# Performance work log

Hardware: AMD Instinct MI355X
Metric: run time of the kernel (lower is better)

## Reference

```python
import jax, jax.numpy as jnp
import numpy as np

B, N, L, ND = 512, 4096, 128, 1


def setup_inputs() -> dict:
    key = jax.random.key(0)
    ks = jax.random.split(key, 20)
    g = lambda k, shape, s=0.05: jax.random.normal(k, shape, dtype=jnp.float32) * s
    IN = 3 * L + ND  # MLP input: [mem, mem, delta_t, x]
    inp = {
        "x": jax.random.normal(ks[0], (B, N, ND), jnp.float32),
        "memory": jax.random.normal(ks[1], (N, L), jnp.float32),
        "delta_t": jax.random.normal(ks[2], (B, N, L), jnp.float32),
        "src_w1": g(ks[3], (L, IN)), "src_b1": g(ks[4], (L,)),
        "src_w2": g(ks[5], (L, L)), "src_b2": g(ks[6], (L,)),
        "tar_w1": g(ks[7], (L, IN)), "tar_b1": g(ks[8], (L,)),
        "tar_w2": g(ks[9], (L, L)), "tar_b2": g(ks[10], (L,)),
        "gru_wih": g(ks[11], (3 * L, L)), "gru_whh": g(ks[12], (3 * L, L)),
        "gru_bih": g(ks[13], (3 * L,)), "gru_bhh": g(ks[14], (3 * L,)),
        "source": jax.random.randint(ks[15], (B, 1), 0, N, dtype=jnp.int64),
        "target": jax.random.randint(ks[16], (B, 1), 0, N, dtype=jnp.int64),
    }
    return inp


def _mlp(h, w1, b1, w2, b2):
    return jax.nn.relu(h @ w1.T + b1) @ w2.T + b2


def _gru_cell(inp, h, wih, whh, bih, bhh):
    gi = inp @ wih.T + bih          # [n, 3L]
    gh = h @ whh.T + bhh            # [n, 3L]
    i_r, i_z, i_n = jnp.split(gi, 3, axis=-1)
    h_r, h_z, h_n = jnp.split(gh, 3, axis=-1)
    r = jax.nn.sigmoid(i_r + h_r)
    z = jax.nn.sigmoid(i_z + h_z)
    n = jnp.tanh(i_n + r * h_n)
    return (1.0 - z) * n + z * h


def reference(x, memory, delta_t, src_w1, src_b1, src_w2, src_b2,
              tar_w1, tar_b1, tar_w2, tar_b2,
              gru_wih, gru_whh, gru_bih, gru_bhh, source, target):
    b = x.shape[0]
    bi = jnp.arange(b)
    s = source[:, 0]
    t = target[:, 0]
    src_mem = memory[s]                 # [B, L]
    tar_mem = memory[t]                 # [B, L]
    src_x = x[bi, s, :]                 # [B, ND]
    tar_x = x[bi, t, :]
    src_dt = delta_t[bi, s, :]          # [B, L]
    tar_dt = delta_t[bi, t, :]
    src_in = jnp.concatenate([src_mem, tar_mem, src_dt, src_x], axis=-1)
    tar_in = jnp.concatenate([tar_mem, src_mem, tar_dt, tar_x], axis=-1)
    src_msg = _mlp(src_in, src_w1, src_b1, src_w2, src_b2)
    tar_msg = _mlp(tar_in, tar_w1, tar_b1, tar_w2, tar_b2)

    # unique + scatter_mean == segment-mean over node ids, touching only seen nodes
    ids = jnp.concatenate([s, t], axis=0)                       # [2B]
    msgs = jnp.concatenate([src_msg, tar_msg], axis=0)          # [2B, L]
    n_nodes = memory.shape[0]
    msg_sum = jax.ops.segment_sum(msgs, ids, num_segments=n_nodes)
    cnt = jax.ops.segment_sum(jnp.ones((ids.shape[0],), msgs.dtype), ids,
                              num_segments=n_nodes)
    agg = msg_sum / jnp.maximum(cnt, 1.0)[:, None]              # [N, L]
    new_mem = _gru_cell(agg, memory, gru_wih, gru_whh, gru_bih, gru_bhh)
    seen = (cnt > 0)[:, None]
    return jnp.where(seen, new_mem, memory)
```

## Files before the change

### kernel.cpp

```cpp
#include <hip/hip_runtime.h>
#include <math.h>

#define BB 512
#define NN 4096
#define LL 128
#define IN_DIM 385
#define IN_PAD 388
#define NK4_1 97
#define NK4_2 32
#define EPB 2
#define GPB 4

#define OFF_MSG   0
#define OFF_CNT   (OFF_MSG + NN * LL)
#define OFF_COUNT (OFF_CNT + NN)
#define OFF_LIST  (OFF_COUNT + 4)
#define OFF_W1PS  529416
#define OFF_W1PT  (OFF_W1PS + NK4_1 * LL * 4)
#define OFF_W2PS  (OFF_W1PT + NK4_1 * LL * 4)
#define OFF_W2PT  (OFF_W2PS + NK4_2 * LL * 4)
#define OFF_WIHP  (OFF_W2PT + NK4_2 * LL * 4)
#define OFF_WHHP  (OFF_WIHP + 3 * NK4_2 * LL * 4)

__global__ __launch_bounds__(256) void prep_kernel(
    const float* __restrict__ memory,
    const float* __restrict__ sw1, const float* __restrict__ tw1,
    const float* __restrict__ sw2, const float* __restrict__ tw2,
    const float* __restrict__ wih, const float* __restrict__ whh,
    float* __restrict__ ws, float* __restrict__ out)
{
    const int i = blockIdx.x * 256 + threadIdx.x;
    const int stride = gridDim.x * 256;

    float4* out4 = (float4*)out;
    const float4* mem4 = (const float4*)memory;
    float4* msg4 = (float4*)(ws + OFF_MSG);
    const float4 z4 = make_float4(0.f, 0.f, 0.f, 0.f);
    for (int idx = i; idx < NN * LL / 4; idx += stride) {
        out4[idx] = mem4[idx];
        msg4[idx] = z4;
    }
    for (int idx = i; idx < NN; idx += stride)
        ws[OFF_CNT + idx] = 0.0f;
    if (i == 0)
        ((int*)ws)[OFF_COUNT] = 0;

    float4* w1ps = (float4*)(ws + OFF_W1PS);
    float4* w1pt = (float4*)(ws + OFF_W1PT);
    for (int idx = i; idx < NK4_1 * LL; idx += stride) {
        const int k4 = idx >> 7, j = idx & 127;
        const int k = k4 * 4;
        float4 a, b;
        a.x = sw1[j * IN_DIM + k];     b.x = tw1[j * IN_DIM + k];
        a.y = sw1[j * IN_DIM + k + 1]; b.y = tw1[j * IN_DIM + k + 1];
        a.z = sw1[j * IN_DIM + k + 2]; b.z = tw1[j * IN_DIM + k + 2];
        if (k + 3 < IN_DIM) { a.w = sw1[j * IN_DIM + k + 3]; b.w = tw1[j * IN_DIM + k + 3]; }
        else                { a.w = 0.f; b.w = 0.f; }
        if (k + 2 >= IN_DIM) { a.z = 0.f; b.z = 0.f; }
        if (k + 1 >= IN_DIM) { a.y = 0.f; b.y = 0.f; }
        w1ps[idx] = a; w1pt[idx] = b;
    }
    float4* w2ps = (float4*)(ws + OFF_W2PS);
    float4* w2pt = (float4*)(ws + OFF_W2PT);
    for (int idx = i; idx < NK4_2 * LL; idx += stride) {
        const int k4 = idx >> 7, j = idx & 127;
        const int k = k4 * 4;
        w2ps[idx] = make_float4(sw2[j * LL + k], sw2[j * LL + k + 1],
                                sw2[j * LL + k + 2], sw2[j * LL + k + 3]);
        w2pt[idx] = make_float4(tw2[j * LL + k], tw2[j * LL + k + 1],
                                tw2[j * LL + k + 2], tw2[j * LL + k + 3]);
    }
    float4* wihp = (float4*)(ws + OFF_WIHP);
    float4* whhp = (float4*)(ws + OFF_WHHP);
    for (int idx = i; idx < 3 * NK4_2 * LL; idx += stride) {
        const int j = idx & 127;
        const int gk = idx >> 7;
        const int gate = gk >> 5, k4 = gk & 31;
        const int row = gate * LL + j, k = k4 * 4;
        wihp[idx] = make_float4(wih[row * LL + k], wih[row * LL + k + 1],
                                wih[row * LL + k + 2], wih[row * LL + k + 3]);
        whhp[idx] = make_float4(whh[row * LL + k], whh[row * LL + k + 1],
                                whh[row * LL + k + 2], whh[row * LL + k + 3]);
    }
}

__global__ __launch_bounds__(256) void edge_msg_kernel(
    const float* __restrict__ x,
    const float* __restrict__ memory,
    const float* __restrict__ delta_t,
    const float* __restrict__ sb1, const float* __restrict__ sb2,
    const float* __restrict__ tb1, const float* __restrict__ tb2,
    const int* __restrict__ source, const int* __restrict__ target,
    float* __restrict__ ws)
{
    const int side  = blockIdx.x & 1;
    const int chunk = blockIdx.x >> 1;
    const int tid   = threadIdx.x;
    const int g     = tid >> 7;
    const int j     = tid & 127;

    __shared__ float in2[IN_PAD][EPB];
    __shared__ float h1[LL][EPB];
    __shared__ float part1[2][EPB][LL];
    __shared__ float part2[2][EPB][LL];
    __shared__ int   node_sh[EPB];

    const float4* w1p = (const float4*)(ws + (side ? OFF_W1PT : OFF_W1PS));
    const float4* w2p = (const float4*)(ws + (side ? OFF_W2PT : OFF_W2PS));
    const float* b1  = side ? tb1 : sb1;
    const float* b2  = side ? tb2 : sb2;

    #pragma unroll
    for (int e = 0; e < EPB; ++e) {
        const int eg = chunk * EPB + e;
        const int s = source[eg], t = target[eg];
        const int node  = side ? t : s;
        const int other = side ? s : t;
        if (tid == 0) node_sh[e] = node;
        for (int idx = tid; idx < IN_PAD; idx += 256) {
            float v = 0.0f;
            if (idx < LL)           v = memory[node * LL + idx];
            else if (idx < 2 * LL)  v = memory[other * LL + (idx - LL)];
            else if (idx < 3 * LL)  v = delta_t[((size_t)eg * NN + node) * LL + (idx - 2 * LL)];
            else if (idx == 3 * LL) v = x[(size_t)eg * NN + node];
            in2[idx][e] = v;
        }
    }
    __syncthreads();

    {
        const int k40 = g ? 49 : 0;
        const int k41 = g ? NK4_1 : 49;
        float a0 = 0.f, a1 = 0.f;
        #pragma unroll 4
        for (int k4 = k40; k4 < k41; ++k4) {
            const float4 w  = w1p[k4 * LL + j];
            const float4 i0 = *(const float4*)&in2[k4 * 4][0];
            const float4 i1 = *(const float4*)&in2[k4 * 4 + 2][0];
            a0 = fmaf(w.x, i0.x, a0); a1 = fmaf(w.x, i0.y, a1);
            a0 = fmaf(w.y, i0.z, a0); a1 = fmaf(w.y, i0.w, a1);
            a0 = fmaf(w.z, i1.x, a0); a1 = fmaf(w.z, i1.y, a1);
            a0 = fmaf(w.w, i1.z, a0); a1 = fmaf(w.w, i1.w, a1);
        }
        part1[g][0][j] = a0;
        part1[g][1][j] = a1;
    }
    __syncthreads();

    h1[j][g] = fmaxf(part1[0][g][j] + part1[1][g][j] + b1[j], 0.0f);
    __syncthreads();

    {
        const int k40 = g * 16, k41 = k40 + 16;
        float a0 = 0.f, a1 = 0.f;
        #pragma unroll 4
        for (int k4 = k40; k4 < k41; ++k4) {
            const float4 w  = w2p[k4 * LL + j];
            const float4 h0 = *(const float4*)&h1[k4 * 4][0];
            const float4 h2 = *(const float4*)&h1[k4 * 4 + 2][0];
            a0 = fmaf(w.x, h0.x, a0); a1 = fmaf(w.x, h0.y, a1);
            a0 = fmaf(w.y, h0.z, a0); a1 = fmaf(w.y, h0.w, a1);
            a0 = fmaf(w.z, h2.x, a0); a1 = fmaf(w.z, h2.y, a1);
            a0 = fmaf(w.w, h2.z, a0); a1 = fmaf(w.w, h2.w, a1);
        }
        part2[g][0][j] = a0;
        part2[g][1][j] = a1;
    }
    __syncthreads();

    {
        const float m = part2[0][g][j] + part2[1][g][j] + b2[j];
        atomicAdd(ws + OFF_MSG + node_sh[g] * LL + j, m);
    }
    if (tid < EPB) {
        const int node = node_sh[tid];
        const float old = atomicAdd(ws + OFF_CNT + node, 1.0f);
        if (old == 0.0f) {
            const int pos = atomicAdd((int*)ws + OFF_COUNT, 1);
            ((int*)ws)[OFF_LIST + pos] = node;
        }
    }
}

__global__ __launch_bounds__(256) void gru_kernel(
    const float* __restrict__ memory,
    const float* __restrict__ bih, const float* __restrict__ bhh,
    float* __restrict__ ws, float* __restrict__ out)
{
    const int tid = threadIdx.x;
    const int g = tid >> 7, j = tid & 127;
    const int scount = ((const int*)ws)[OFF_COUNT];
    const int base = blockIdx.x * GPB;
    if (base >= scount) return;
    const int nact = min(GPB, scount - base);

    __shared__ float ah[LL][2 * GPB];
    __shared__ float gates[6][GPB][LL];
    __shared__ int   nodes_sh[GPB];

    if (tid < GPB)
        nodes_sh[tid] = (base + tid < scount)
                        ? ((const int*)ws)[OFF_LIST + base + tid] : -1;
    __syncthreads();

    #pragma unroll
    for (int gi = 0; gi < GPB; ++gi) {
        const int node = nodes_sh[gi];
        if (g == 0) {
            float v = 0.0f;
            if (node >= 0) {
                const float c = ws[OFF_CNT + node];
                v = ws[OFF_MSG + node * LL + j] / c;
            }
            ah[j][gi] = v;
        } else {
            ah[j][GPB + gi] = (node >= 0) ? memory[node * LL + j] : 0.0f;
        }
    }
    __syncthreads();

    const float4* wp = (const float4*)(ws + (g ? OFF_WHHP : OFF_WIHP));
    float a0[GPB] = {}, a1[GPB] = {}, a2[GPB] = {};
    #pragma unroll 2
    for (int k4 = 0; k4 < NK4_2; ++k4) {
        const float4 w0 = wp[(0 * NK4_2 + k4) * LL + j];
        const float4 w1 = wp[(1 * NK4_2 + k4) * LL + j];
        const float4 w2 = wp[(2 * NK4_2 + k4) * LL + j];
        const float w0a[4] = {w0.x, w0.y, w0.z, w0.w};
        const float w1a[4] = {w1.x, w1.y, w1.z, w1.w};
        const float w2a[4] = {w2.x, w2.y, w2.z, w2.w};
        #pragma unroll
        for (int c = 0; c < 4; ++c) {
            const float4 v4 = *(const float4*)&ah[k4 * 4 + c][g * GPB];
            const float va[4] = {v4.x, v4.y, v4.z, v4.w};
            #pragma unroll
            for (int gi = 0; gi < GPB; ++gi) {
                a0[gi] = fmaf(w0a[c], va[gi], a0[gi]);
                a1[gi] = fmaf(w1a[c], va[gi], a1[gi]);
                a2[gi] = fmaf(w2a[c], va[gi], a2[gi]);
            }
        }
    }
    #pragma unroll
    for (int gi = 0; gi < GPB; ++gi) {
        gates[g * 3 + 0][gi][j] = a0[gi];
        gates[g * 3 + 1][gi][j] = a1[gi];
        gates[g * 3 + 2][gi][j] = a2[gi];
    }
    __syncthreads();

    const int total = nact * LL;
    for (int o = tid; o < total; o += 256) {
        const int gi = o >> 7, jj = o & 127;
        const int node = nodes_sh[gi];
        const float ir = gates[0][gi][jj] + bih[jj];
        const float iz = gates[1][gi][jj] + bih[LL + jj];
        const float inn = gates[2][gi][jj] + bih[2 * LL + jj];
        const float hr = gates[3][gi][jj] + bhh[jj];
        const float hz = gates[4][gi][jj] + bhh[LL + jj];
        const float hn = gates[5][gi][jj] + bhh[2 * LL + jj];
        const float r = 1.0f / (1.0f + __expf(-(ir + hr)));
        const float z = 1.0f / (1.0f + __expf(-(iz + hz)));
        const float n = tanhf(inn + r * hn);
        const float h = ah[jj][GPB + gi];
        out[node * LL + jj] = (1.0f - z) * n + z * h;
    }
}

extern "C" void kernel_launch(void* const* d_in, const int* in_sizes, int n_in,
                              void* d_out, int out_size, void* d_ws, size_t ws_size,
                              hipStream_t stream) {
    const float* x        = (const float*)d_in[0];
    const float* memory   = (const float*)d_in[1];
    const float* delta_t  = (const float*)d_in[2];
    const float* src_w1   = (const float*)d_in[3];
    const float* src_b1   = (const float*)d_in[4];
    const float* src_w2   = (const float*)d_in[5];
    const float* src_b2   = (const float*)d_in[6];
    const float* tar_w1   = (const float*)d_in[7];
    const float* tar_b1   = (const float*)d_in[8];
    const float* tar_w2   = (const float*)d_in[9];
    const float* tar_b2   = (const float*)d_in[10];
    const float* gru_wih  = (const float*)d_in[11];
    const float* gru_whh  = (const float*)d_in[12];
    const float* gru_bih  = (const float*)d_in[13];
    const float* gru_bhh  = (const float*)d_in[14];
    const int*   source   = (const int*)d_in[15];
    const int*   target   = (const int*)d_in[16];

    float* out = (float*)d_out;
    float* ws  = (float*)d_ws;

    prep_kernel<<<512, 256, 0, stream>>>(
        memory, src_w1, tar_w1, src_w2, tar_w2, gru_wih, gru_whh, ws, out);

    edge_msg_kernel<<<2 * (BB / EPB), 256, 0, stream>>>(
        x, memory, delta_t, src_b1, src_b2, tar_b1, tar_b2,
        source, target, ws);

    gru_kernel<<<1024 / GPB, 256, 0, stream>>>(
        memory, gru_bih, gru_bhh, ws, out);
}
```

Baseline: 36.93 us.

## Replace atomic scatter-mean with per-task messages and in-block duplicate grouping

Edge messages are now written to a per-task buffer with their node ids, instead of being atomically added into a zeroed N×L accumulator. The GRU kernel now finds, for each task, all tasks with the same node id by scanning the node list in shared memory. It averages them in index order, and only the first occurrence of a node writes the output. This removes the large memset of the message accumulator, the count and list atomics, and the pre-packing of W2 and the GRU weights, which are now read directly from row-major global memory. The memory-to-output copy moves into extra blocks of the edge kernel. In exchange, every GRU block redundantly scans all 1024 node ids, duplicate nodes repeat the GRU compute, and the unpacked weight reads are less coalesced.

```diff
diff --git a/kernel.cpp b/kernel.cpp
--- a/kernel.cpp
+++ b/kernel.cpp
@@ -7,43 +7,21 @@
 #define IN_DIM 385
 #define IN_PAD 388
 #define NK4_1 97
-#define NK4_2 32
 #define EPB 2
+#define TASKS 1024
 #define GPB 4
 
-#define OFF_MSG   0
-#define OFF_CNT   (OFF_MSG + NN * LL)
-#define OFF_COUNT (OFF_CNT + NN)
-#define OFF_LIST  (OFF_COUNT + 4)
-#define OFF_W1PS  529416
+#define OFF_MSGS  0
+#define OFF_NODES (OFF_MSGS + TASKS * LL)
+#define OFF_W1PS  (OFF_NODES + TASKS)
 #define OFF_W1PT  (OFF_W1PS + NK4_1 * LL * 4)
-#define OFF_W2PS  (OFF_W1PT + NK4_1 * LL * 4)
-#define OFF_W2PT  (OFF_W2PS + NK4_2 * LL * 4)
-#define OFF_WIHP  (OFF_W2PT + NK4_2 * LL * 4)
-#define OFF_WHHP  (OFF_WIHP + 3 * NK4_2 * LL * 4)
 
 __global__ __launch_bounds__(256) void prep_kernel(
-    const float* __restrict__ memory,
     const float* __restrict__ sw1, const float* __restrict__ tw1,
-    const float* __restrict__ sw2, const float* __restrict__ tw2,
-    const float* __restrict__ wih, const float* __restrict__ whh,
-    float* __restrict__ ws, float* __restrict__ out)
+    float* __restrict__ ws)
 {
     const int i = blockIdx.x * 256 + threadIdx.x;
     const int stride = gridDim.x * 256;
-
-    float4* out4 = (float4*)out;
-    const float4* mem4 = (const float4*)memory;
-    float4* msg4 = (float4*)(ws + OFF_MSG);
-    const float4 z4 = make_float4(0.f, 0.f, 0.f, 0.f);
-    for (int idx = i; idx < NN * LL / 4; idx += stride) {
-        out4[idx] = mem4[idx];
-        msg4[idx] = z4;
-    }
-    for (int idx = i; idx < NN; idx += stride)
-        ws[OFF_CNT + idx] = 0.0f;
-    if (i == 0)
-        ((int*)ws)[OFF_COUNT] = 0;
 
     float4* w1ps = (float4*)(ws + OFF_W1PS);
     float4* w1pt = (float4*)(ws + OFF_W1PT);
@@ -52,35 +30,13 @@
         const int k = k4 * 4;
         float4 a, b;
         a.x = sw1[j * IN_DIM + k];     b.x = tw1[j * IN_DIM + k];
-        a.y = sw1[j * IN_DIM + k + 1]; b.y = tw1[j * IN_DIM + k + 1];
-        a.z = sw1[j * IN_DIM + k + 2]; b.z = tw1[j * IN_DIM + k + 2];
-        if (k + 3 < IN_DIM) { a.w = sw1[j * IN_DIM + k + 3]; b.w = tw1[j * IN_DIM + k + 3]; }
-        else                { a.w = 0.f; b.w = 0.f; }
-        if (k + 2 >= IN_DIM) { a.z = 0.f; b.z = 0.f; }
-        if (k + 1 >= IN_DIM) { a.y = 0.f; b.y = 0.f; }
+        a.y = (k + 1 < IN_DIM) ? sw1[j * IN_DIM + k + 1] : 0.f;
+        b.y = (k + 1 < IN_DIM) ? tw1[j * IN_DIM + k + 1] : 0.f;
+        a.z = (k + 2 < IN_DIM) ? sw1[j * IN_DIM + k + 2] : 0.f;
+        b.z = (k + 2 < IN_DIM) ? tw1[j * IN_DIM + k + 2] : 0.f;
+        a.w = (k + 3 < IN_DIM) ? sw1[j * IN_DIM + k + 3] : 0.f;
+        b.w = (k + 3 < IN_DIM) ? tw1[j * IN_DIM + k + 3] : 0.f;
         w1ps[idx] = a; w1pt[idx] = b;
-    }
-    float4* w2ps = (float4*)(ws + OFF_W2PS);
-    float4* w2pt = (float4*)(ws + OFF_W2PT);
-    for (int idx = i; idx < NK4_2 * LL; idx += stride) {
-        const int k4 = idx >> 7, j = idx & 127;
-        const int k = k4 * 4;
-        w2ps[idx] = make_float4(sw2[j * LL + k], sw2[j * LL + k + 1],
-                                sw2[j * LL + k + 2], sw2[j * LL + k + 3]);
-        w2pt[idx] = make_float4(tw2[j * LL + k], tw2[j * LL + k + 1],
-                                tw2[j * LL + k + 2], tw2[j * LL + k + 3]);
-    }
-    float4* wihp = (float4*)(ws + OFF_WIHP);
-    float4* whhp = (float4*)(ws + OFF_WHHP);
-    for (int idx = i; idx < 3 * NK4_2 * LL; idx += stride) {
-        const int j = idx & 127;
-        const int gk = idx >> 7;
-        const int gate = gk >> 5, k4 = gk & 31;
-        const int row = gate * LL + j, k = k4 * 4;
-        wihp[idx] = make_float4(wih[row * LL + k], wih[row * LL + k + 1],
-                                wih[row * LL + k + 2], wih[row * LL + k + 3]);
-        whhp[idx] = make_float4(whh[row * LL + k], whh[row * LL + k + 1],
-                                whh[row * LL + k + 2], whh[row * LL + k + 3]);
     }
 }
 
@@ -88,14 +44,26 @@
     const float* __restrict__ x,
     const float* __restrict__ memory,
     const float* __restrict__ delta_t,
-    const float* __restrict__ sb1, const float* __restrict__ sb2,
-    const float* __restrict__ tb1, const float* __restrict__ tb2,
+    const float* __restrict__ sb1, const float* __restrict__ sw2,
+    const float* __restrict__ sb2,
+    const float* __restrict__ tb1, const float* __restrict__ tw2,
+    const float* __restrict__ tb2,
     const int* __restrict__ source, const int* __restrict__ target,
-    float* __restrict__ ws)
+    float* __restrict__ ws, float* __restrict__ out)
 {
+    const int tid = threadIdx.x;
+
+    if (blockIdx.x >= 512) {
+        const int cb = blockIdx.x - 512;
+        float4* out4 = (float4*)out;
+        const float4* mem4 = (const float4*)memory;
+        for (int idx = cb * 256 + tid; idx < NN * LL / 4; idx += 32 * 256)
+            out4[idx] = mem4[idx];
+        return;
+    }
+
     const int side  = blockIdx.x & 1;
     const int chunk = blockIdx.x >> 1;
-    const int tid   = threadIdx.x;
     const int g     = tid >> 7;
     const int j     = tid & 127;
 
@@ -106,7 +74,7 @@
     __shared__ int   node_sh[EPB];
 
     const float4* w1p = (const float4*)(ws + (side ? OFF_W1PT : OFF_W1PS));
-    const float4* w2p = (const float4*)(ws + (side ? OFF_W2PT : OFF_W2PS));
+    const float* w2  = side ? tw2 : sw2;
     const float* b1  = side ? tb1 : sb1;
     const float* b2  = side ? tb2 : sb2;
 
@@ -151,17 +119,18 @@
     __syncthreads();
 
     {
-        const int k40 = g * 16, k41 = k40 + 16;
+        const int k0 = g * 64;
         float a0 = 0.f, a1 = 0.f;
         #pragma unroll 4
-        for (int k4 = k40; k4 < k41; ++k4) {
-            const float4 w  = w2p[k4 * LL + j];
-            const float4 h0 = *(const float4*)&h1[k4 * 4][0];
-            const float4 h2 = *(const float4*)&h1[k4 * 4 + 2][0];
-            a0 = fmaf(w.x, h0.x, a0); a1 = fmaf(w.x, h0.y, a1);
-            a0 = fmaf(w.y, h0.z, a0); a1 = fmaf(w.y, h0.w, a1);
-            a0 = fmaf(w.z, h2.x, a0); a1 = fmaf(w.z, h2.y, a1);
-            a0 = fmaf(w.w, h2.z, a0); a1 = fmaf(w.w, h2.w, a1);
+        for (int i = 0; i < 16; ++i) {
+            const int k = k0 + 4 * i;
+            const float4 w  = *(const float4*)&w2[j * LL + k];
+            const float4 hA = *(const float4*)&h1[k][0];
+            const float4 hB = *(const float4*)&h1[k + 2][0];
+            a0 = fmaf(w.x, hA.x, a0); a1 = fmaf(w.x, hA.y, a1);
+            a0 = fmaf(w.y, hA.z, a0); a1 = fmaf(w.y, hA.w, a1);
+            a0 = fmaf(w.z, hB.x, a0); a1 = fmaf(w.z, hB.y, a1);
+            a0 = fmaf(w.w, hB.z, a0); a1 = fmaf(w.w, hB.w, a1);
         }
         part2[g][0][j] = a0;
         part2[g][1][j] = a1;
@@ -170,62 +139,85 @@
 
     {
         const float m = part2[0][g][j] + part2[1][g][j] + b2[j];
-        atomicAdd(ws + OFF_MSG + node_sh[g] * LL + j, m);
-    }
-    if (tid < EPB) {
-        const int node = node_sh[tid];
-        const float old = atomicAdd(ws + OFF_CNT + node, 1.0f);
-        if (old == 0.0f) {
-            const int pos = atomicAdd((int*)ws + OFF_COUNT, 1);
-            ((int*)ws)[OFF_LIST + pos] = node;
-        }
+        const int task = side * BB + chunk * EPB + g;
+        ws[OFF_MSGS + task * LL + j] = m;
+        if (j == 0)
+            ((int*)ws)[OFF_NODES + task] = node_sh[g];
     }
 }
 
 __global__ __launch_bounds__(256) void gru_kernel(
     const float* __restrict__ memory,
+    const float* __restrict__ wih, const float* __restrict__ whh,
     const float* __restrict__ bih, const float* __restrict__ bhh,
     float* __restrict__ ws, float* __restrict__ out)
 {
     const int tid = threadIdx.x;
     const int g = tid >> 7, j = tid & 127;
-    const int scount = ((const int*)ws)[OFF_COUNT];
-    const int base = blockIdx.x * GPB;
-    if (base >= scount) return;
-    const int nact = min(GPB, scount - base);
-
+
+    __shared__ int   snodes[TASKS];
+    __shared__ int   matches[GPB][TASKS];
+    __shared__ int   cnt_sh[GPB];
+    __shared__ int   nd_sh[GPB];
     __shared__ float ah[LL][2 * GPB];
     __shared__ float gates[6][GPB][LL];
-    __shared__ int   nodes_sh[GPB];
+
+    const int* nodes_arr = (const int*)ws + OFF_NODES;
+
+    for (int e = tid; e < TASKS; e += 256)
+        snodes[e] = nodes_arr[e];
+    if (tid < GPB) cnt_sh[tid] = 0;
+    __syncthreads();
 
     if (tid < GPB)
-        nodes_sh[tid] = (base + tid < scount)
-                        ? ((const int*)ws)[OFF_LIST + base + tid] : -1;
+        nd_sh[tid] = snodes[blockIdx.x * GPB + tid];
+    __syncthreads();
+
+    for (int e = tid; e < TASKS; e += 256) {
+        const int ne = snodes[e];
+        #pragma unroll
+        for (int s = 0; s < GPB; ++s) {
+            if (ne == nd_sh[s]) {
+                const int p = atomicAdd(&cnt_sh[s], 1);
+                matches[s][p] = e;
+            }
+        }
+    }
+    __syncthreads();
+
+    if (tid < GPB) {
+        const int c = cnt_sh[tid];
+        int* m = matches[tid];
+        for (int a = 1; a < c; ++a) {
+            const int v = m[a];
+            int b = a - 1;
+            while (b >= 0 && m[b] > v) { m[b + 1] = m[b]; --b; }
+            m[b + 1] = v;
+        }
+    }
     __syncthreads();
 
     #pragma unroll
-    for (int gi = 0; gi < GPB; ++gi) {
-        const int node = nodes_sh[gi];
+    for (int s = 0; s < GPB; ++s) {
         if (g == 0) {
-            float v = 0.0f;
-            if (node >= 0) {
-                const float c = ws[OFF_CNT + node];
-                v = ws[OFF_MSG + node * LL + j] / c;
-            }
-            ah[j][gi] = v;
+            const int c = cnt_sh[s];
+            float a = 0.0f;
+            for (int m = 0; m < c; ++m)
+                a += ws[OFF_MSGS + matches[s][m] * LL + j];
+            ah[j][s] = a / (float)c;
         } else {
-            ah[j][GPB + gi] = (node >= 0) ? memory[node * LL + j] : 0.0f;
-        }
-    }
-    __syncthreads();
-
-    const float4* wp = (const float4*)(ws + (g ? OFF_WHHP : OFF_WIHP));
+            ah[j][GPB + s] = memory[nd_sh[s] * LL + j];
+        }
+    }
+    __syncthreads();
+
+    const float* wmat = g ? whh : wih;
     float a0[GPB] = {}, a1[GPB] = {}, a2[GPB] = {};
     #pragma unroll 2
-    for (int k4 = 0; k4 < NK4_2; ++k4) {
-        const float4 w0 = wp[(0 * NK4_2 + k4) * LL + j];
-        const float4 w1 = wp[(1 * NK4_2 + k4) * LL + j];
-        const float4 w2 = wp[(2 * NK4_2 + k4) * LL + j];
+    for (int k4 = 0; k4 < 32; ++k4) {
+        const float4 w0 = *(const float4*)&wmat[(0 * LL + j) * LL + 4 * k4];
+        const float4 w1 = *(const float4*)&wmat[(1 * LL + j) * LL + 4 * k4];
+        const float4 w2 = *(const float4*)&wmat[(2 * LL + j) * LL + 4 * k4];
         const float w0a[4] = {w0.x, w0.y, w0.z, w0.w};
         const float w1a[4] = {w1.x, w1.y, w1.z, w1.w};
         const float w2a[4] = {w2.x, w2.y, w2.z, w2.w};
@@ -234,36 +226,36 @@
             const float4 v4 = *(const float4*)&ah[k4 * 4 + c][g * GPB];
             const float va[4] = {v4.x, v4.y, v4.z, v4.w};
             #pragma unroll
-            for (int gi = 0; gi < GPB; ++gi) {
-                a0[gi] = fmaf(w0a[c], va[gi], a0[gi]);
-                a1[gi] = fmaf(w1a[c], va[gi], a1[gi]);
-                a2[gi] = fmaf(w2a[c], va[gi], a2[gi]);
+            for (int s = 0; s < GPB; ++s) {
+                a0[s] = fmaf(w0a[c], va[s], a0[s]);
+                a1[s] = fmaf(w1a[c], va[s], a1[s]);
+                a2[s] = fmaf(w2a[c], va[s], a2[s]);
             }
         }
     }
     #pragma unroll
-    for (int gi = 0; gi < GPB; ++gi) {
-        gates[g * 3 + 0][gi][j] = a0[gi];
-        gates[g * 3 + 1][gi][j] = a1[gi];
-        gates[g * 3 + 2][gi][j] = a2[gi];
-    }
-    __syncthreads();
-
-    const int total = nact * LL;
-    for (int o = tid; o < total; o += 256) {
-        const int gi = o >> 7, jj = o & 127;
-        const int node = nodes_sh[gi];
-        const float ir = gates[0][gi][jj] + bih[jj];
-        const float iz = gates[1][gi][jj] + bih[LL + jj];
-        const float inn = gates[2][gi][jj] + bih[2 * LL + jj];
-        const float hr = gates[3][gi][jj] + bhh[jj];
-        const float hz = gates[4][gi][jj] + bhh[LL + jj];
-        const float hn = gates[5][gi][jj] + bhh[2 * LL + jj];
+    for (int s = 0; s < GPB; ++s) {
+        gates[g * 3 + 0][s][j] = a0[s];
+        gates[g * 3 + 1][s][j] = a1[s];
+        gates[g * 3 + 2][s][j] = a2[s];
+    }
+    __syncthreads();
+
+    for (int o = tid; o < GPB * LL; o += 256) {
+        const int s = o >> 7, jj = o & 127;
+        const int task = blockIdx.x * GPB + s;
+        if (matches[s][0] != task) continue;
+        const float ir = gates[0][s][jj] + bih[jj];
+        const float iz = gates[1][s][jj] + bih[LL + jj];
+        const float inn = gates[2][s][jj] + bih[2 * LL + jj];
+        const float hr = gates[3][s][jj] + bhh[jj];
+        const float hz = gates[4][s][jj] + bhh[LL + jj];
+        const float hn = gates[5][s][jj] + bhh[2 * LL + jj];
         const float r = 1.0f / (1.0f + __expf(-(ir + hr)));
         const float z = 1.0f / (1.0f + __expf(-(iz + hz)));
         const float n = tanhf(inn + r * hn);
-        const float h = ah[jj][GPB + gi];
-        out[node * LL + jj] = (1.0f - z) * n + z * h;
+        const float h = ah[jj][GPB + s];
+        out[nd_sh[s] * LL + jj] = (1.0f - z) * n + z * h;
     }
 }
 
@@ -291,13 +283,13 @@
     float* out = (float*)d_out;
     float* ws  = (float*)d_ws;
 
-    prep_kernel<<<512, 256, 0, stream>>>(
-        memory, src_w1, tar_w1, src_w2, tar_w2, gru_wih, gru_whh, ws, out);
-
-    edge_msg_kernel<<<2 * (BB / EPB), 256, 0, stream>>>(
-        x, memory, delta_t, src_b1, src_b2, tar_b1, tar_b2,
-        source, target, ws);
-
-    gru_kernel<<<1024 / GPB, 256, 0, stream>>>(
-        memory, gru_bih, gru_bhh, ws, out);
-}
+    prep_kernel<<<256, 256, 0, stream>>>(src_w1, tar_w1, ws);
+
+    edge_msg_kernel<<<544, 256, 0, stream>>>(
+        x, memory, delta_t,
+        src_b1, src_w2, src_b2, tar_b1, tar_w2, tar_b2,
+        source, target, ws, out);
+
+    gru_kernel<<<TASKS / GPB, 256, 0, stream>>>(
+        memory, gru_wih, gru_whh, gru_bih, gru_bhh, ws, out);
+}
```

New measurement: 40.85 us. +10.6%, slower.
